# Optimization experiments

Hardware: AMD Instinct MI355X
Metric: run time of the kernel (lower is better)

The kernel has to match this reference:

```python
import jax, jax.numpy as jnp
import numpy as np

NEG_SLOPE = 0.01  # nn.LeakyReLU default

N = 100000
E = 1600000
D_IN = 128
D_OUT = 128


def setup_inputs() -> dict:
    key = jax.random.key(0)
    ks = jax.random.split(key, 8)
    features = jax.random.normal(ks[0], (N, D_IN), dtype=jnp.float32)
    adj_rows = jax.random.randint(ks[1], (E,), 0, N, dtype=jnp.int64)
    adj_cols = jax.random.randint(ks[2], (E,), 0, N, dtype=jnp.int64)
    adj_vals = jax.random.uniform(ks[3], (E,), dtype=jnp.float32)
    s1 = 1.0 / np.sqrt(D_IN)
    W1 = jax.random.uniform(ks[4], (D_IN, D_OUT), jnp.float32, -s1, s1)
    b1 = jax.random.uniform(ks[5], (D_OUT,), jnp.float32, -s1, s1)
    W2 = jax.random.uniform(ks[6], (D_IN, D_OUT), jnp.float32, -s1, s1)
    b2 = jax.random.uniform(ks[7], (D_OUT,), jnp.float32, -s1, s1)
    return {"features": features, "adj_rows": adj_rows, "adj_cols": adj_cols,
            "adj_vals": adj_vals, "W1": W1, "b1": b1, "W2": W2, "b2": b2}


def reference(features, adj_rows, adj_cols, adj_vals, W1, b1, W2, b2):
    # h_neigh = adj @ features  (COO SpMM via gather + segment_sum)
    msgs = adj_vals[:, None] * features[adj_cols]          # [E, D_IN]
    h_neigh = jax.ops.segment_sum(msgs, adj_rows, num_segments=features.shape[0])
    term1 = (features + h_neigh) @ W1 + b1                 # W1(features + h_neigh)
    term2 = (features * h_neigh) @ W2 + b2                 # W2(features * h_neigh)
    pre = term1 + term2
    return jnp.where(pre >= 0, pre, NEG_SLOPE * pre)       # leaky_relu
```

## Files before the change

### kernel.cpp

```cpp
#include <hip/hip_runtime.h>

#define D 128
#define BM 64

typedef short short8 __attribute__((ext_vector_type(8)));
typedef unsigned short ushort8_t __attribute__((ext_vector_type(8)));
typedef float f32x4 __attribute__((ext_vector_type(4)));

__device__ __forceinline__ unsigned short f2bf(float x) {
    unsigned u = __float_as_uint(x);
    unsigned r = (u + 0x7fffu + ((u >> 16) & 1u)) >> 16;
    return (unsigned short)r;
}
__device__ __forceinline__ float bf2f(unsigned short u) {
    return __uint_as_float(((unsigned)u) << 16);
}

__global__ __launch_bounds__(256) void fconv_kernel(
    const float4* __restrict__ feat4, ushort4* __restrict__ fbf4, int total)
{
    int i = blockIdx.x * 256 + threadIdx.x;
    if (i < total) {
        float4 v = feat4[i];
        fbf4[i] = make_ushort4(f2bf(v.x), f2bf(v.y), f2bf(v.z), f2bf(v.w));
    }
}

__global__ __launch_bounds__(256) void wconv_kernel(
    const float* __restrict__ W1, const float* __restrict__ W2,
    unsigned short* __restrict__ WT)
{
    int idx = blockIdx.x * 256 + threadIdx.x;
    int c = idx & 127;
    int k = idx >> 7;
    float w = (k < 128) ? W1[k * 128 + c] : W2[(k - 128) * 128 + c];
    WT[c * 256 + k] = f2bf(w);
}


__global__ __launch_bounds__(256) void bucket_hist_kernel(
    const int* __restrict__ rows, int* __restrict__ bcnt, int E, int nb, int epb)
{
    __shared__ int cnt[1024];
    int t = threadIdx.x;
    for (int i = t; i < nb; i += 256) cnt[i] = 0;
    __syncthreads();
    int e0 = blockIdx.x * epb;
    int e1 = e0 + epb; if (e1 > E) e1 = E;
    for (int e = e0 + t; e < e1; e += 256) atomicAdd(&cnt[rows[e] >> 7], 1);
    __syncthreads();
    for (int i = t; i < nb; i += 256)
        if (cnt[i]) atomicAdd(&bcnt[i], cnt[i]);
}

__global__ __launch_bounds__(1024) void bucket_scan_kernel(
    const int* __restrict__ bcnt, int* __restrict__ bstart,
    int* __restrict__ bcur, int nb, int E)
{
    __shared__ int wsum[16];
    int tid = threadIdx.x, lane = tid & 63, wid = tid >> 6;
    int x = (tid < nb) ? bcnt[tid] : 0;
    int v = x;
    #pragma unroll
    for (int off = 1; off < 64; off <<= 1) {
        int y = __shfl_up(v, off, 64);
        if (lane >= off) v += y;
    }
    if (lane == 63) wsum[wid] = v;
    __syncthreads();
    if (wid == 0 && lane < 16) {
        int s = wsum[lane];
        #pragma unroll
        for (int off = 1; off < 16; off <<= 1) {
            int y = __shfl_up(s, off, 64);
            if (lane >= off) s += y;
        }
        wsum[lane] = s;
    }
    __syncthreads();
    int wexcl = wid ? wsum[wid - 1] : 0;
    int excl = wexcl + v - x;
    if (tid < nb) { bstart[tid] = excl; bcur[tid] = excl; }
    if (tid == 0) bstart[nb] = E;
}

__global__ __launch_bounds__(256) void bucket_scatter_kernel(
    const int* __restrict__ rows, const int* __restrict__ cols,
    const float* __restrict__ vals, int* __restrict__ bcur,
    uint2* __restrict__ bsedge, int E, int nb)
{
    __shared__ int cnt[1024];
    __shared__ int base[1024];
    int t = threadIdx.x;
    int e0 = blockIdx.x * 4096;
    for (int i = t; i < nb; i += 256) cnt[i] = 0;
    __syncthreads();
    #pragma unroll
    for (int q = 0; q < 16; ++q) {
        int e = e0 + t + q * 256;
        if (e < E) atomicAdd(&cnt[rows[e] >> 7], 1);
    }
    __syncthreads();
    for (int i = t; i < nb; i += 256) {
        int c = cnt[i];
        if (c) { base[i] = atomicAdd(&bcur[i], c); cnt[i] = 0; }
    }
    __syncthreads();
    #pragma unroll
    for (int q = 0; q < 16; ++q) {
        int e = e0 + t + q * 256;
        if (e < E) {
            int r = rows[e];
            int b = r >> 7;
            int pos = base[b] + atomicAdd(&cnt[b], 1);
            bsedge[pos] = make_uint2(((unsigned)(r & 127) << 17) | (unsigned)cols[e],
                                     __float_as_uint(vals[e]));
        }
    }
}

__global__ __launch_bounds__(256) void bucket_sort_kernel(
    const uint2* __restrict__ bsedge,
    const int* __restrict__ bstart,
    uint2* __restrict__ sedge,
    int* __restrict__ row_start,
    int N, int E)
{
    __shared__ int cnt[128];
    __shared__ int base[128];
    const int b = blockIdx.x;
    const int t = threadIdx.x;
    const int s = bstart[b], e = bstart[b + 1];
    if (t < 128) cnt[t] = 0;
    __syncthreads();
    for (int j = s + t; j < e; j += 256)
        atomicAdd(&cnt[bsedge[j].x >> 17], 1);
    __syncthreads();
    if (t < 64) {
        int c0 = cnt[2 * t], c1 = cnt[2 * t + 1];
        int pair = c0 + c1;
        int v = pair;
        #pragma unroll
        for (int off = 1; off < 64; off <<= 1) {
            int y = __shfl_up(v, off, 64);
            if (t >= off) v += y;
        }
        int excl = v - pair;
        base[2 * t]     = excl;
        base[2 * t + 1] = excl + c0;
        cnt[2 * t] = 0;
        cnt[2 * t + 1] = 0;
    }
    __syncthreads();
    const int r0 = b << 7;
    if (t < 128 && r0 + t < N) row_start[r0 + t] = s + base[t];
    if (b == 0 && t == 0) row_start[N] = E;
    for (int j = s + t; j < e; j += 256) {
        uint2 ed = bsedge[j];
        int rl = ed.x >> 17;
        int p = atomicAdd(&cnt[rl], 1);
        sedge[s + base[rl] + p] = make_uint2(ed.x & 0x1FFFFu, ed.y);
    }
}

__global__ __launch_bounds__(256) void spmm_ab_kernel(
    const float4* __restrict__ feat4,
    const ushort8_t* __restrict__ fbf8,
    const int* __restrict__ row_start,
    const uint2* __restrict__ sedge,
    unsigned char* __restrict__ ambf, int N)
{
    int t = blockIdx.x * 256 + threadIdx.x;
    int row = t >> 4;
    int l   = t & 15;
    if (row >= N) return;

    int s = row_start[row];
    int e = row_start[row + 1];

    float acc[8] = {};
    int j = s;
    for (; j + 1 < e; j += 2) {
        uint2 e0 = sedge[j], e1 = sedge[j + 1];
        float v0 = __uint_as_float(e0.y), v1 = __uint_as_float(e1.y);
        ushort8_t f0 = fbf8[(size_t)e0.x * 16 + l];
        ushort8_t f1 = fbf8[(size_t)e1.x * 16 + l];
        #pragma unroll
        for (int q = 0; q < 8; ++q) {
            acc[q] = fmaf(v0, bf2f(f0[q]), acc[q]);
            acc[q] = fmaf(v1, bf2f(f1[q]), acc[q]);
        }
    }
    if (j < e) {
        uint2 e0 = sedge[j];
        float v = __uint_as_float(e0.y);
        ushort8_t f = fbf8[(size_t)e0.x * 16 + l];
        #pragma unroll
        for (int q = 0; q < 8; ++q) acc[q] = fmaf(v, bf2f(f[q]), acc[q]);
    }

    float4 fa = feat4[(size_t)row * 32 + 2 * l];
    float4 fb = feat4[(size_t)row * 32 + 2 * l + 1];
    float f[8] = { fa.x, fa.y, fa.z, fa.w, fb.x, fb.y, fb.z, fb.w };

    ushort8_t av, mv;
    #pragma unroll
    for (int q = 0; q < 8; ++q) {
        av[q] = f2bf(f[q] + acc[q]);
        mv[q] = f2bf(f[q] * acc[q]);
    }

    int swz = (row & 7) << 4;
    unsigned char* rowp = ambf + (size_t)row * 512;
    *(ushort8_t*)(rowp + ((16 * l) ^ swz))       = av;
    *(ushort8_t*)(rowp + 256 + ((16 * l) ^ swz)) = mv;
}

__global__ __launch_bounds__(256) void mfma_gemm2_kernel(
    const unsigned char* __restrict__ ambf,
    const unsigned short* __restrict__ WT,
    const float* __restrict__ b1, const float* __restrict__ b2,
    float* __restrict__ out, int N)
{
    __shared__ __align__(16) unsigned char am_raw[64 * 512];

    const int tid = threadIdx.x;
    const int block0 = blockIdx.x * BM;

    const short8* src = (const short8*)(ambf + (size_t)block0 * 512);
    short8* dst = (short8*)am_raw;
    #pragma unroll
    for (int it = 0; it < 8; ++it) {
        int idx = tid + it * 256;
        dst[idx] = src[idx];
    }
    __syncthreads();

    const int lane = tid & 63;
    const int w    = tid >> 6;
    const int wr   = w >> 1;
    const int wc   = w & 1;
    const int l15  = lane & 15;
    const int lk   = lane >> 4;
    const int rswz = (l15 & 7) << 4;

    f32x4 acc[2][4] = {};

    const char* WTc = (const char*)WT;
    const unsigned char* arow0 = am_raw + (wr * 32 + l15) * 512;
    const unsigned char* arow1 = arow0 + 16 * 512;

    #pragma unroll
    for (int ks = 0; ks < 8; ++ks) {
        int kbyte = ks * 64 + lk * 16;
        int akoff = kbyte ^ rswz;
        short8 a0 = *(const short8*)(arow0 + akoff);
        short8 a1 = *(const short8*)(arow1 + akoff);
        short8 bfr[4];
        #pragma unroll
        for (int nc = 0; nc < 4; ++nc) {
            int col = wc * 64 + nc * 16 + l15;
            bfr[nc] = *(const short8*)(WTc + col * 512 + kbyte);
        }
        #pragma unroll
        for (int nc = 0; nc < 4; ++nc) {
            acc[0][nc] = __builtin_amdgcn_mfma_f32_16x16x32_bf16(a0, bfr[nc], acc[0][nc], 0, 0, 0);
            acc[1][nc] = __builtin_amdgcn_mfma_f32_16x16x32_bf16(a1, bfr[nc], acc[1][nc], 0, 0, 0);
        }
    }

    #pragma unroll
    for (int nc = 0; nc < 4; ++nc) {
        int col = wc * 64 + nc * 16 + l15;
        float bias = b1[col] + b2[col];
        #pragma unroll
        for (int mr = 0; mr < 2; ++mr) {
            int rbase = block0 + wr * 32 + mr * 16 + lk * 4;
            #pragma unroll
            for (int r = 0; r < 4; ++r) {
                int row = rbase + r;
                if (row < N) {
                    float v = acc[mr][nc][r] + bias;
                    out[row * 128 + col] = (v >= 0.f) ? v : 0.01f * v;
                }
            }
        }
    }
}

__global__ __launch_bounds__(256) void hist_kernel(
    const int* __restrict__ rows, int* __restrict__ counts, int E)
{
    int e = blockIdx.x * 256 + threadIdx.x;
    if (e < E) atomicAdd(&counts[rows[e]], 1);
}

__global__ __launch_bounds__(256) void scan_pass1(
    const int* __restrict__ counts, int* __restrict__ btot, int N)
{
    int tid = threadIdx.x;
    int i = blockIdx.x * 1024 + tid * 4;
    int s = 0;
    if (i + 3 < N) {
        int4 v = *(const int4*)(counts + i);
        s = v.x + v.y + v.z + v.w;
    } else {
        for (int q = 0; q < 4; ++q) if (i + q < N) s += counts[i + q];
    }
    #pragma unroll
    for (int off = 32; off >= 1; off >>= 1) s += __shfl_down(s, off, 64);
    __shared__ int ws[4];
    if ((tid & 63) == 0) ws[tid >> 6] = s;
    __syncthreads();
    if (tid == 0) btot[blockIdx.x] = ws[0] + ws[1] + ws[2] + ws[3];
}

__global__ __launch_bounds__(1024) void scan_pass2(
    const int* __restrict__ btot, int* __restrict__ boff, int nb)
{
    __shared__ int wsum[16];
    int tid = threadIdx.x, lane = tid & 63, wid = tid >> 6;
    int x = (tid < nb) ? btot[tid] : 0;
    int v = x;
    #pragma unroll
    for (int off = 1; off < 64; off <<= 1) {
        int y = __shfl_up(v, off, 64);
        if (lane >= off) v += y;
    }
    if (lane == 63) wsum[wid] = v;
    __syncthreads();
    if (wid == 0 && lane < 16) {
        int s = wsum[lane];
        #pragma unroll
        for (int off = 1; off < 16; off <<= 1) {
            int y = __shfl_up(s, off, 64);
            if (lane >= off) s += y;
        }
        wsum[lane] = s;
    }
    __syncthreads();
    int wexcl = wid ? wsum[wid - 1] : 0;
    if (tid < nb) boff[tid] = wexcl + v - x;
}

__global__ __launch_bounds__(256) void scan_pass3(
    int* __restrict__ row_start, int* __restrict__ cursor,
    const int* __restrict__ boff, int N, int E)
{
    int tid = threadIdx.x;
    int base = blockIdx.x * 1024 + tid * 4;
    int c0 = 0, c1 = 0, c2 = 0, c3 = 0;
    if (base + 3 < N) {
        int4 v = *(const int4*)(row_start + base);
        c0 = v.x; c1 = v.y; c2 = v.z; c3 = v.w;
    } else {
        if (base + 0 < N) c0 = row_start[base + 0];
        if (base + 1 < N) c1 = row_start[base + 1];
        if (base + 2 < N) c2 = row_start[base + 2];
        if (base + 3 < N) c3 = row_start[base + 3];
    }
    int s0 = c0, s1 = s0 + c1, s2 = s1 + c2, s3 = s2 + c3;
    int lane = tid & 63, wid = tid >> 6;
    int v = s3;
    #pragma unroll
    for (int off = 1; off < 64; off <<= 1) {
        int y = __shfl_up(v, off, 64);
        if (lane >= off) v += y;
    }
    __shared__ int ws[4];
    if (lane == 63) ws[wid] = v;
    __syncthreads();
    int wexcl = 0;
    for (int q = 0; q < wid; ++q) wexcl += ws[q];
    int texcl = wexcl + (v - s3) + boff[blockIdx.x];
    int e0 = texcl, e1 = texcl + s0, e2 = texcl + s1, e3 = texcl + s2;
    if (base + 0 < N) { row_start[base + 0] = e0; cursor[base + 0] = e0; }
    if (base + 1 < N) { row_start[base + 1] = e1; cursor[base + 1] = e1; }
    if (base + 2 < N) { row_start[base + 2] = e2; cursor[base + 2] = e2; }
    if (base + 3 < N) { row_start[base + 3] = e3; cursor[base + 3] = e3; }
    if (blockIdx.x == 0 && tid == 0) row_start[N] = E;
}

__global__ __launch_bounds__(256) void scatter_sort_kernel(
    const int* __restrict__ rows, const int* __restrict__ cols,
    const float* __restrict__ vals, int* __restrict__ cursor,
    uint2* __restrict__ sedge, int E)
{
    int e = blockIdx.x * 256 + threadIdx.x;
    if (e < E) {
        int r = rows[e];
        int p = atomicAdd(&cursor[r], 1);
        sedge[p] = make_uint2((unsigned)cols[e], __float_as_uint(vals[e]));
    }
}

__global__ __launch_bounds__(256) void spmm_kernel(
    const float2* __restrict__ feat2,
    const int* __restrict__ row_start,
    const uint2* __restrict__ sedge,
    float2* __restrict__ h2, int N)
{
    int gw = (blockIdx.x * 256 + threadIdx.x) >> 6;
    int lane = threadIdx.x & 63;
    if (gw >= N) return;
    int s = row_start[gw];
    int e = row_start[gw + 1];
    float2 acc = make_float2(0.f, 0.f);
    int j = s;
    for (; j + 1 < e; j += 2) {
        uint2 e0 = sedge[j], e1 = sedge[j + 1];
        float v0 = __uint_as_float(e0.y), v1 = __uint_as_float(e1.y);
        float2 f0 = feat2[(size_t)e0.x * 64 + lane];
        float2 f1 = feat2[(size_t)e1.x * 64 + lane];
        acc.x = fmaf(v0, f0.x, acc.x);
        acc.y = fmaf(v0, f0.y, acc.y);
        acc.x = fmaf(v1, f1.x, acc.x);
        acc.y = fmaf(v1, f1.y, acc.y);
    }
    if (j < e) {
        uint2 e0 = sedge[j];
        float v = __uint_as_float(e0.y);
        float2 f = feat2[(size_t)e0.x * 64 + lane];
        acc.x = fmaf(v, f.x, acc.x);
        acc.y = fmaf(v, f.y, acc.y);
    }
    h2[(size_t)gw * 64 + lane] = acc;
}

__global__ __launch_bounds__(256) void mfma_gemm_kernel(
    const float4* __restrict__ feat4, const float4* __restrict__ h4,
    const unsigned short* __restrict__ WT,
    const float* __restrict__ b1, const float* __restrict__ b2,
    float* __restrict__ out, int N)
{
    __shared__ __align__(16) unsigned char am_raw[64 * 512];
    const int tid = threadIdx.x;
    const int block0 = blockIdx.x * BM;
    #pragma unroll
    for (int it = 0; it < 8; ++it) {
        int idx  = tid + it * 256;
        int node = idx >> 5;
        int p    = idx & 31;
        int g    = block0 + node;
        float4 fv = make_float4(0.f, 0.f, 0.f, 0.f);
        float4 hv = make_float4(0.f, 0.f, 0.f, 0.f);
        if (g < N) { fv = feat4[g * 32 + p]; hv = h4[g * 32 + p]; }
        ushort4 av = make_ushort4(f2bf(fv.x + hv.x), f2bf(fv.y + hv.y),
                                  f2bf(fv.z + hv.z), f2bf(fv.w + hv.w));
        ushort4 mv = make_ushort4(f2bf(fv.x * hv.x), f2bf(fv.y * hv.y),
                                  f2bf(fv.z * hv.z), f2bf(fv.w * hv.w));
        int swz = (node & 7) << 4;
        *(ushort4*)(am_raw + node * 512 + ((p * 8) ^ swz))       = av;
        *(ushort4*)(am_raw + node * 512 + ((256 + p * 8) ^ swz)) = mv;
    }
    __syncthreads();
    const int lane = tid & 63;
    const int w    = tid >> 6;
    const int wr   = w >> 1;
    const int wc   = w & 1;
    const int l15  = lane & 15;
    const int lk   = lane >> 4;
    const int rswz = (l15 & 7) << 4;
    f32x4 acc[2][4] = {};
    const char* WTc = (const char*)WT;
    const unsigned char* arow0 = am_raw + (wr * 32 + l15) * 512;
    const unsigned char* arow1 = arow0 + 16 * 512;
    #pragma unroll
    for (int ks = 0; ks < 8; ++ks) {
        int kbyte = ks * 64 + lk * 16;
        int akoff = kbyte ^ rswz;
        short8 a0 = *(const short8*)(arow0 + akoff);
        short8 a1 = *(const short8*)(arow1 + akoff);
        short8 bfr[4];
        #pragma unroll
        for (int nc = 0; nc < 4; ++nc) {
            int col = wc * 64 + nc * 16 + l15;
            bfr[nc] = *(const short8*)(WTc + col * 512 + kbyte);
        }
        #pragma unroll
        for (int nc = 0; nc < 4; ++nc) {
            acc[0][nc] = __builtin_amdgcn_mfma_f32_16x16x32_bf16(a0, bfr[nc], acc[0][nc], 0, 0, 0);
            acc[1][nc] = __builtin_amdgcn_mfma_f32_16x16x32_bf16(a1, bfr[nc], acc[1][nc], 0, 0, 0);
        }
    }
    #pragma unroll
    for (int nc = 0; nc < 4; ++nc) {
        int col = wc * 64 + nc * 16 + l15;
        float bias = b1[col] + b2[col];
        #pragma unroll
        for (int mr = 0; mr < 2; ++mr) {
            int rbase = block0 + wr * 32 + mr * 16 + lk * 4;
            #pragma unroll
            for (int r = 0; r < 4; ++r) {
                int row = rbase + r;
                if (row < N) {
                    float v = acc[mr][nc][r] + bias;
                    out[row * 128 + col] = (v >= 0.f) ? v : 0.01f * v;
                }
            }
        }
    }
}

__global__ __launch_bounds__(256) void edge_scatter_kernel(
    const float4* __restrict__ feat4, const int* __restrict__ rows,
    const int* __restrict__ cols, const float* __restrict__ vals,
    float* __restrict__ h, int E)
{
    int idx = blockIdx.x * 256 + threadIdx.x;
    if (idx >= E * 32) return;
    int e = idx >> 5;
    int p = idx & 31;
    int r = rows[e];
    int c = cols[e];
    float v = vals[e];
    float4 f = feat4[c * 32 + p];
    float* hr = h + (long long)r * D + p * 4;
    unsafeAtomicAdd(hr + 0, v * f.x);
    unsafeAtomicAdd(hr + 1, v * f.y);
    unsafeAtomicAdd(hr + 2, v * f.z);
    unsafeAtomicAdd(hr + 3, v * f.w);
}

__global__ __launch_bounds__(256) void fused_gemm_kernel(
    const float* __restrict__ feat, const float* __restrict__ h,
    const float* __restrict__ W1, const float* __restrict__ b1,
    const float* __restrict__ W2, const float* __restrict__ b2,
    float* __restrict__ out, int N)
{
    __shared__ float a_lds[BM][D];
    __shared__ float m_lds[BM][D];
    const int tid = threadIdx.x;
    const int block0 = blockIdx.x * BM;
    const float4* feat4 = (const float4*)feat;
    const float4* h4    = (const float4*)h;
    #pragma unroll
    for (int it = 0; it < 8; ++it) {
        int idx  = tid + it * 256;
        int node = idx >> 5;
        int p    = idx & 31;
        int gnode = block0 + node;
        float4 fv = make_float4(0.f, 0.f, 0.f, 0.f);
        float4 hv = make_float4(0.f, 0.f, 0.f, 0.f);
        if (gnode < N) { fv = feat4[gnode * 32 + p]; hv = h4[gnode * 32 + p]; }
        float4 av = make_float4(fv.x + hv.x, fv.y + hv.y, fv.z + hv.z, fv.w + hv.w);
        float4 mv = make_float4(fv.x * hv.x, fv.y * hv.y, fv.z * hv.z, fv.w * hv.w);
        *(float4*)&a_lds[node][p * 4] = av;
        *(float4*)&m_lds[node][p * 4] = mv;
    }
    __syncthreads();
    const int c = tid & 31;
    const int g = tid >> 5;
    float acc[8][4] = {};
    const float4* W1v = (const float4*)W1;
    const float4* W2v = (const float4*)W2;
    for (int k = 0; k < D; ++k) {
        float4 w1 = W1v[k * 32 + c];
        float4 w2 = W2v[k * 32 + c];
        #pragma unroll
        for (int t = 0; t < 8; ++t) {
            float av = a_lds[g + 8 * t][k];
            float mv = m_lds[g + 8 * t][k];
            acc[t][0] = fmaf(av, w1.x, fmaf(mv, w2.x, acc[t][0]));
            acc[t][1] = fmaf(av, w1.y, fmaf(mv, w2.y, acc[t][1]));
            acc[t][2] = fmaf(av, w1.z, fmaf(mv, w2.z, acc[t][2]));
            acc[t][3] = fmaf(av, w1.w, fmaf(mv, w2.w, acc[t][3]));
        }
    }
    float4 bb1 = ((const float4*)b1)[c];
    float4 bb2 = ((const float4*)b2)[c];
    const float bx = bb1.x + bb2.x, by = bb1.y + bb2.y;
    const float bz = bb1.z + bb2.z, bw = bb1.w + bb2.w;
    #pragma unroll
    for (int t = 0; t < 8; ++t) {
        int gnode = block0 + g + 8 * t;
        if (gnode >= N) continue;
        float4 o;
        o.x = acc[t][0] + bx; o.y = acc[t][1] + by;
        o.z = acc[t][2] + bz; o.w = acc[t][3] + bw;
        o.x = (o.x >= 0.f) ? o.x : 0.01f * o.x;
        o.y = (o.y >= 0.f) ? o.y : 0.01f * o.y;
        o.z = (o.z >= 0.f) ? o.z : 0.01f * o.z;
        o.w = (o.w >= 0.f) ? o.w : 0.01f * o.w;
        ((float4*)out)[gnode * 32 + c] = o;
    }
}

extern "C" void kernel_launch(void* const* d_in, const int* in_sizes, int n_in,
                              void* d_out, int out_size, void* d_ws, size_t ws_size,
                              hipStream_t stream) {
    const float* feat = (const float*)d_in[0];
    const int*   rows = (const int*)d_in[1];
    const int*   cols = (const int*)d_in[2];
    const float* vals = (const float*)d_in[3];
    const float* W1   = (const float*)d_in[4];
    const float* b1   = (const float*)d_in[5];
    const float* W2   = (const float*)d_in[6];
    const float* b2   = (const float*)d_in[7];

    const int N = in_sizes[0] / D;
    const int E = in_sizes[1];
    float* out = (float*)d_out;

    const int NBK  = (N + 127) >> 7;
    const int Npad = NBK << 7;

    size_t off = 0;
    unsigned char* ambf = (unsigned char*)d_ws;                    off += (size_t)Npad * 512;
    unsigned short* featbf = (unsigned short*)((char*)d_ws + off); off += (size_t)N * D * 2;
    off = (off + 15) & ~(size_t)15;
    uint2* sedge = (uint2*)((char*)d_ws + off);                    off += (size_t)E * 8;
    unsigned short* WT = (unsigned short*)((char*)d_ws + off);     off += 128 * 256 * 2;
    int* row_start = (int*)((char*)d_ws + off);                    off += (size_t)(N + 1) * 4;
    size_t common = off;

    off = (common + 15) & ~(size_t)15;
    uint2* bsedge = (uint2*)((char*)d_ws + off);                   off += (size_t)E * 8;
    int* bcnt   = (int*)((char*)d_ws + off);                       off += (size_t)NBK * 4;
    int* bstart = (int*)((char*)d_ws + off);                       off += (size_t)(NBK + 1) * 4;
    int* bcur   = (int*)((char*)d_ws + off);                       off += (size_t)NBK * 4;
    size_t need1a = off;

    if (ws_size >= need1a && NBK <= 1024 && N <= (1 << 17)) {
        hipMemsetAsync(bcnt, 0, (size_t)NBK * sizeof(int), stream);
        fconv_kernel<<<(N * 32 + 255) / 256, 256, 0, stream>>>(
            (const float4*)feat, (ushort4*)featbf, N * 32);
        wconv_kernel<<<128, 256, 0, stream>>>(W1, W2, WT);
        int epb = (E + 255) / 256;
        bucket_hist_kernel<<<256, 256, 0, stream>>>(rows, bcnt, E, NBK, epb);
        bucket_scan_kernel<<<1, 1024, 0, stream>>>(bcnt, bstart, bcur, NBK, E);
        bucket_scatter_kernel<<<(E + 4095) / 4096, 256, 0, stream>>>(
            rows, cols, vals, bcur, bsedge, E, NBK);
        bucket_sort_kernel<<<NBK, 256, 0, stream>>>(
            bsedge, bstart, sedge, row_start, N, E);
        spmm_ab_kernel<<<(N * 16 + 255) / 256, 256, 0, stream>>>(
            (const float4*)feat, (const ushort8_t*)featbf, row_start, sedge,
            ambf, N);
        mfma_gemm2_kernel<<<(N + BM - 1) / BM, 256, 0, stream>>>(
            ambf, WT, b1, b2, out, N);
        return;
    }

    const int NB = (N + 1023) / 1024;
    off = (common + 15) & ~(size_t)15;
    int* cursor = (int*)((char*)d_ws + off);                       off += (size_t)N * 4;
    int* btot = (int*)((char*)d_ws + off);                         off += (size_t)NB * 4;
    int* boff = (int*)((char*)d_ws + off);                         off += (size_t)NB * 4;
    size_t need1b = off;

    if (ws_size >= need1b && NB <= 1024) {
        hipMemsetAsync(row_start, 0, (size_t)(N + 1) * sizeof(int), stream);
        fconv_kernel<<<(N * 32 + 255) / 256, 256, 0, stream>>>(
            (const float4*)feat, (ushort4*)featbf, N * 32);
        wconv_kernel<<<128, 256, 0, stream>>>(W1, W2, WT);
        hist_kernel<<<(E + 255) / 256, 256, 0, stream>>>(rows, row_start, E);
        scan_pass1<<<NB, 256, 0, stream>>>(row_start, btot, N);
        scan_pass2<<<1, 1024, 0, stream>>>(btot, boff, NB);
        scan_pass3<<<NB, 256, 0, stream>>>(row_start, cursor, boff, N, E);
        scatter_sort_kernel<<<(E + 255) / 256, 256, 0, stream>>>(
            rows, cols, vals, cursor, sedge, E);
        spmm_ab_kernel<<<(N * 16 + 255) / 256, 256, 0, stream>>>(
            (const float4*)feat, (const ushort8_t*)featbf, row_start, sedge,
            ambf, N);
        mfma_gemm2_kernel<<<(N + BM - 1) / BM, 256, 0, stream>>>(
            ambf, WT, b1, b2, out, N);
        return;
    }

    off = 0;
    float* h = (float*)d_ws;                           off += (size_t)N * D * 4;
    int* row_start2 = (int*)((char*)d_ws + off);       off += (size_t)(N + 1) * 4;
    int* cursor2    = (int*)((char*)d_ws + off);       off += (size_t)N * 4;
    off = (off + 15) & ~(size_t)15;
    uint2* sedge2   = (uint2*)((char*)d_ws + off);     off += (size_t)E * 8;
    off = (off + 15) & ~(size_t)15;
    unsigned short* WT2 = (unsigned short*)((char*)d_ws + off); off += 128 * 256 * 2;
    int* btot2 = (int*)((char*)d_ws + off);            off += (size_t)NB * 4;
    int* boff2 = (int*)((char*)d_ws + off);            off += (size_t)NB * 4;
    size_t need2 = off;

    if (ws_size >= need2 && NB <= 1024) {
        hipMemsetAsync(row_start2, 0, (size_t)(N + 1) * sizeof(int), stream);
        wconv_kernel<<<128, 256, 0, stream>>>(W1, W2, WT2);
        hist_kernel<<<(E + 255) / 256, 256, 0, stream>>>(rows, row_start2, E);
        scan_pass1<<<NB, 256, 0, stream>>>(row_start2, btot2, N);
        scan_pass2<<<1, 1024, 0, stream>>>(btot2, boff2, NB);
        scan_pass3<<<NB, 256, 0, stream>>>(row_start2, cursor2, boff2, N, E);
        scatter_sort_kernel<<<(E + 255) / 256, 256, 0, stream>>>(
            rows, cols, vals, cursor2, sedge2, E);
        spmm_kernel<<<(N * 64 + 255) / 256, 256, 0, stream>>>(
            (const float2*)feat, row_start2, sedge2, (float2*)h, N);
        mfma_gemm_kernel<<<(N + BM - 1) / BM, 256, 0, stream>>>(
            (const float4*)feat, (const float4*)h, WT2, b1, b2, out, N);
        return;
    }

    size_t hbytes = (size_t)N * D * sizeof(float);
    float* hh = (ws_size >= hbytes) ? (float*)d_ws : out;
    hipMemsetAsync(hh, 0, hbytes, stream);
    edge_scatter_kernel<<<((size_t)E * 32 + 255) / 256, 256, 0, stream>>>(
        (const float4*)feat, rows, cols, vals, hh, E);
    fused_gemm_kernel<<<(N + BM - 1) / BM, 256, 0, stream>>>(
        feat, hh, W1, b1, W2, b2, out, N);
}
```

Measured before the change: 200.4 us.

## Fuse SpMM aggregation with MFMA GEMM epilogue through shared memory

```diff
diff --git a/kernel.cpp b/kernel.cpp
--- a/kernel.cpp
+++ b/kernel.cpp
@@ -160,6 +160,125 @@
         int rl = ed.x >> 17;
         int p = atomicAdd(&cnt[rl], 1);
         sedge[s + base[rl] + p] = make_uint2(ed.x & 0x1FFFFu, ed.y);
+    }
+}
+
+__global__ __launch_bounds__(256) void spmm_gemm_kernel(
+    const float4* __restrict__ feat4,
+    const ushort8_t* __restrict__ fbf8,
+    const int* __restrict__ row_start,
+    const uint2* __restrict__ sedge,
+    const unsigned short* __restrict__ WT,
+    const float* __restrict__ b1, const float* __restrict__ b2,
+    float* __restrict__ out, int N)
+{
+    __shared__ __align__(16) unsigned char am_raw[64 * 512];
+
+    const int tid = threadIdx.x;
+    const int block0 = blockIdx.x * BM;
+    const int rq = tid >> 4;
+    const int l  = tid & 15;
+
+    for (int it = 0; it < 4; ++it) {
+        int node = it * 16 + rq;
+        int row = block0 + node;
+        float acc[8] = {};
+        float f[8] = {};
+        if (row < N) {
+            int s = row_start[row];
+            int e = row_start[row + 1];
+            int j = s;
+            for (; j + 3 < e; j += 4) {
+                uint2 e0 = sedge[j],     e1 = sedge[j + 1];
+                uint2 e2 = sedge[j + 2], e3 = sedge[j + 3];
+                ushort8_t f0 = fbf8[(size_t)e0.x * 16 + l];
+                ushort8_t f1 = fbf8[(size_t)e1.x * 16 + l];
+                ushort8_t f2 = fbf8[(size_t)e2.x * 16 + l];
+                ushort8_t f3 = fbf8[(size_t)e3.x * 16 + l];
+                float v0 = __uint_as_float(e0.y), v1 = __uint_as_float(e1.y);
+                float v2 = __uint_as_float(e2.y), v3 = __uint_as_float(e3.y);
+                #pragma unroll
+                for (int q = 0; q < 8; ++q) {
+                    acc[q] = fmaf(v0, bf2f(f0[q]), acc[q]);
+                    acc[q] = fmaf(v1, bf2f(f1[q]), acc[q]);
+                    acc[q] = fmaf(v2, bf2f(f2[q]), acc[q]);
+                    acc[q] = fmaf(v3, bf2f(f3[q]), acc[q]);
+                }
+            }
+            for (; j < e; ++j) {
+                uint2 e0 = sedge[j];
+                float v = __uint_as_float(e0.y);
+                ushort8_t f0 = fbf8[(size_t)e0.x * 16 + l];
+                #pragma unroll
+                for (int q = 0; q < 8; ++q) acc[q] = fmaf(v, bf2f(f0[q]), acc[q]);
+            }
+            float4 fa = feat4[(size_t)row * 32 + 2 * l];
+            float4 fb = feat4[(size_t)row * 32 + 2 * l + 1];
+            f[0] = fa.x; f[1] = fa.y; f[2] = fa.z; f[3] = fa.w;
+            f[4] = fb.x; f[5] = fb.y; f[6] = fb.z; f[7] = fb.w;
+        }
+        ushort8_t av, mv;
+        #pragma unroll
+        for (int q = 0; q < 8; ++q) {
+            av[q] = f2bf(f[q] + acc[q]);
+            mv[q] = f2bf(f[q] * acc[q]);
+        }
+        int swz = (node & 7) << 4;
+        unsigned char* rowp = am_raw + node * 512;
+        *(ushort8_t*)(rowp + ((16 * l) ^ swz))       = av;
+        *(ushort8_t*)(rowp + 256 + ((16 * l) ^ swz)) = mv;
+    }
+    __syncthreads();
+
+    const int lane = tid & 63;
+    const int w    = tid >> 6;
+    const int wr   = w >> 1;
+    const int wc   = w & 1;
+    const int l15  = lane & 15;
+    const int lk   = lane >> 4;
+    const int rswz = (l15 & 7) << 4;
+
+    f32x4 gacc[2][4] = {};
+
+    const char* WTc = (const char*)WT;
+    const unsigned char* arow0 = am_raw + (wr * 32 + l15) * 512;
+    const unsigned char* arow1 = arow0 + 16 * 512;
+
+    #pragma unroll
+    for (int ks = 0; ks < 8; ++ks) {
+        int kbyte = ks * 64 + lk * 16;
+        int akoff = kbyte ^ rswz;
+        short8 a0 = *(const short8*)(arow0 + akoff);
+        short8 a1 = *(const short8*)(arow1 + akoff);
+        short8 bfr[4];
+        #pragma unroll
+        for (int nc = 0; nc < 4; ++nc) {
+            int col = wc * 64 + nc * 16 + l15;
+            bfr[nc] = *(const short8*)(WTc + col * 512 + kbyte);
+        }
+        #pragma unroll
+        for (int nc = 0; nc < 4; ++nc) {
+            gacc[0][nc] = __builtin_amdgcn_mfma_f32_16x16x32_bf16(a0, bfr[nc], gacc[0][nc], 0, 0, 0);
+            gacc[1][nc] = __builtin_amdgcn_mfma_f32_16x16x32_bf16(a1, bfr[nc], gacc[1][nc], 0, 0, 0);
+        }
+    }
+
+    #pragma unroll
+    for (int nc = 0; nc < 4; ++nc) {
+        int col = wc * 64 + nc * 16 + l15;
+        float bias = b1[col] + b2[col];
+        #pragma unroll
+        for (int mr = 0; mr < 2; ++mr) {
+            int rbase = block0 + wr * 32 + mr * 16 + lk * 4;
+            #pragma unroll
+            for (int r = 0; r < 4; ++r) {
+                int row = rbase + r;
+                if (row < N) {
+                    float v = gacc[mr][nc][r] + bias;
+                    out[row * 128 + col] = (v >= 0.f) ? v : 0.01f * v;
+                }
+            }
+        }
     }
 }
 
@@ -606,15 +725,12 @@
     const int Npad = NBK << 7;
 
     size_t off = 0;
-    unsigned char* ambf = (unsigned char*)d_ws;                    off += (size_t)Npad * 512;
-    unsigned short* featbf = (unsigned short*)((char*)d_ws + off); off += (size_t)N * D * 2;
+    unsigned short* featbf = (unsigned short*)d_ws;                off += (size_t)N * D * 2;
     off = (off + 15) & ~(size_t)15;
     uint2* sedge = (uint2*)((char*)d_ws + off);                    off += (size_t)E * 8;
     unsigned short* WT = (unsigned short*)((char*)d_ws + off);     off += 128 * 256 * 2;
     int* row_start = (int*)((char*)d_ws + off);                    off += (size_t)(N + 1) * 4;
-    size_t common = off;
-
-    off = (common + 15) & ~(size_t)15;
+    off = (off + 15) & ~(size_t)15;
     uint2* bsedge = (uint2*)((char*)d_ws + off);                   off += (size_t)E * 8;
     int* bcnt   = (int*)((char*)d_ws + off);                       off += (size_t)NBK * 4;
     int* bstart = (int*)((char*)d_ws + off);                       off += (size_t)(NBK + 1) * 4;
@@ -633,16 +749,21 @@
             rows, cols, vals, bcur, bsedge, E, NBK);
         bucket_sort_kernel<<<NBK, 256, 0, stream>>>(
             bsedge, bstart, sedge, row_start, N, E);
-        spmm_ab_kernel<<<(N * 16 + 255) / 256, 256, 0, stream>>>(
+        spmm_gemm_kernel<<<(N + BM - 1) / BM, 256, 0, stream>>>(
             (const float4*)feat, (const ushort8_t*)featbf, row_start, sedge,
-            ambf, N);
-        mfma_gemm2_kernel<<<(N + BM - 1) / BM, 256, 0, stream>>>(
-            ambf, WT, b1, b2, out, N);
+            WT, b1, b2, out, N);
         return;
     }
 
     const int NB = (N + 1023) / 1024;
-    off = (common + 15) & ~(size_t)15;
+    off = 0;
+    unsigned char* ambf = (unsigned char*)d_ws;                    off += (size_t)Npad * 512;
+    featbf = (unsigned short*)((char*)d_ws + off);                 off += (size_t)N * D * 2;
+    off = (off + 15) & ~(size_t)15;
+    sedge = (uint2*)((char*)d_ws + off);                           off += (size_t)E * 8;
+    WT = (unsigned short*)((char*)d_ws + off);                     off += 128 * 256 * 2;
+    row_start = (int*)((char*)d_ws + off);                         off += (size_t)(N + 1) * 4;
+    off = (off + 15) & ~(size_t)15;
     int* cursor = (int*)((char*)d_ws + off);                       off += (size_t)N * 4;
     int* btot = (int*)((char*)d_ws + off);                         off += (size_t)NB * 4;
     int* boff = (int*)((char*)d_ws + off);                         off += (size_t)NB * 4;
```

New measurement: 191.8 us. 1.04x faster.

## Fuse feature/weight conversion with bucket histogram; unroll SpMM gather by four

Applied to the files above, without the earlier changes.

```diff
diff --git a/kernel.cpp b/kernel.cpp
--- a/kernel.cpp
+++ b/kernel.cpp
@@ -14,6 +14,41 @@
 }
 __device__ __forceinline__ float bf2f(unsigned short u) {
     return __uint_as_float(((unsigned)u) << 16);
+}
+
+__global__ __launch_bounds__(256) void prep_kernel(
+    const float4* __restrict__ feat4, ushort4* __restrict__ fbf4, int nf4,
+    const float* __restrict__ W1, const float* __restrict__ W2,
+    unsigned short* __restrict__ WT,
+    const int* __restrict__ rows, int* __restrict__ bcnt,
+    int E, int nb, int epb)
+{
+    __shared__ int cnt[1024];
+    const int t = threadIdx.x;
+    const int b = blockIdx.x;
+    for (int i = t; i < nb; i += 256) cnt[i] = 0;
+    __syncthreads();
+
+    int e0 = b * epb;
+    int e1 = e0 + epb; if (e1 > E) e1 = E;
+    for (int e = e0 + t; e < e1; e += 256) atomicAdd(&cnt[rows[e] >> 7], 1);
+
+    for (int i = b * 256 + t; i < nf4; i += 256 * 256) {
+        float4 v = feat4[i];
+        fbf4[i] = make_ushort4(f2bf(v.x), f2bf(v.y), f2bf(v.z), f2bf(v.w));
+    }
+
+    if (b < 128) {
+        int idx = b * 256 + t;
+        int c = idx & 127;
+        int k = idx >> 7;
+        float w = (k < 128) ? W1[k * 128 + c] : W2[(k - 128) * 128 + c];
+        WT[c * 256 + k] = f2bf(w);
+    }
+
+    __syncthreads();
+    for (int i = t; i < nb; i += 256)
+        if (cnt[i]) atomicAdd(&bcnt[i], cnt[i]);
 }
 
 __global__ __launch_bounds__(256) void fconv_kernel(
@@ -35,22 +70,6 @@
     int k = idx >> 7;
     float w = (k < 128) ? W1[k * 128 + c] : W2[(k - 128) * 128 + c];
     WT[c * 256 + k] = f2bf(w);
-}
-
-
-__global__ __launch_bounds__(256) void bucket_hist_kernel(
-    const int* __restrict__ rows, int* __restrict__ bcnt, int E, int nb, int epb)
-{
-    __shared__ int cnt[1024];
-    int t = threadIdx.x;
-    for (int i = t; i < nb; i += 256) cnt[i] = 0;
-    __syncthreads();
-    int e0 = blockIdx.x * epb;
-    int e1 = e0 + epb; if (e1 > E) e1 = E;
-    for (int e = e0 + t; e < e1; e += 256) atomicAdd(&cnt[rows[e] >> 7], 1);
-    __syncthreads();
-    for (int i = t; i < nb; i += 256)
-        if (cnt[i]) atomicAdd(&bcnt[i], cnt[i]);
 }
 
 __global__ __launch_bounds__(1024) void bucket_scan_kernel(
@@ -164,7 +183,6 @@
 }
 
 __global__ __launch_bounds__(256) void spmm_ab_kernel(
-    const float4* __restrict__ feat4,
     const ushort8_t* __restrict__ fbf8,
     const int* __restrict__ row_start,
     const uint2* __restrict__ sedge,
@@ -180,34 +198,38 @@
 
     float acc[8] = {};
     int j = s;
-    for (; j + 1 < e; j += 2) {
-        uint2 e0 = sedge[j], e1 = sedge[j + 1];
-        float v0 = __uint_as_float(e0.y), v1 = __uint_as_float(e1.y);
+    for (; j + 3 < e; j += 4) {
+        uint2 e0 = sedge[j],     e1 = sedge[j + 1];
+        uint2 e2 = sedge[j + 2], e3 = sedge[j + 3];
         ushort8_t f0 = fbf8[(size_t)e0.x * 16 + l];
         ushort8_t f1 = fbf8[(size_t)e1.x * 16 + l];
+        ushort8_t f2 = fbf8[(size_t)e2.x * 16 + l];
+        ushort8_t f3 = fbf8[(size_t)e3.x * 16 + l];
+        float v0 = __uint_as_float(e0.y), v1 = __uint_as_float(e1.y);
+        float v2 = __uint_as_float(e2.y), v3 = __uint_as_float(e3.y);
         #pragma unroll
         for (int q = 0; q < 8; ++q) {
             acc[q] = fmaf(v0, bf2f(f0[q]), acc[q]);
             acc[q] = fmaf(v1, bf2f(f1[q]), acc[q]);
-        }
-    }
-    if (j < e) {
+            acc[q] = fmaf(v2, bf2f(f2[q]), acc[q]);
+            acc[q] = fmaf(v3, bf2f(f3[q]), acc[q]);
+        }
+    }
+    for (; j < e; ++j) {
         uint2 e0 = sedge[j];
         float v = __uint_as_float(e0.y);
-        ushort8_t f = fbf8[(size_t)e0.x * 16 + l];
-        #pragma unroll
-        for (int q = 0; q < 8; ++q) acc[q] = fmaf(v, bf2f(f[q]), acc[q]);
-    }
-
-    float4 fa = feat4[(size_t)row * 32 + 2 * l];
-    float4 fb = feat4[(size_t)row * 32 + 2 * l + 1];
-    float f[8] = { fa.x, fa.y, fa.z, fa.w, fb.x, fb.y, fb.z, fb.w };
-
+        ushort8_t f0 = fbf8[(size_t)e0.x * 16 + l];
+        #pragma unroll
+        for (int q = 0; q < 8; ++q) acc[q] = fmaf(v, bf2f(f0[q]), acc[q]);
+    }
+
+    ushort8_t fown = fbf8[(size_t)row * 16 + l];
     ushort8_t av, mv;
     #pragma unroll
     for (int q = 0; q < 8; ++q) {
-        av[q] = f2bf(f[q] + acc[q]);
-        mv[q] = f2bf(f[q] * acc[q]);
+        float f = bf2f(fown[q]);
+        av[q] = f2bf(f + acc[q]);
+        mv[q] = f2bf(f * acc[q]);
     }
 
     int swz = (row & 7) << 4;
@@ -612,9 +634,7 @@
     uint2* sedge = (uint2*)((char*)d_ws + off);                    off += (size_t)E * 8;
     unsigned short* WT = (unsigned short*)((char*)d_ws + off);     off += 128 * 256 * 2;
     int* row_start = (int*)((char*)d_ws + off);                    off += (size_t)(N + 1) * 4;
-    size_t common = off;
-
-    off = (common + 15) & ~(size_t)15;
+    off = (off + 15) & ~(size_t)15;
     uint2* bsedge = (uint2*)((char*)d_ws + off);                   off += (size_t)E * 8;
     int* bcnt   = (int*)((char*)d_ws + off);                       off += (size_t)NBK * 4;
     int* bstart = (int*)((char*)d_ws + off);                       off += (size_t)(NBK + 1) * 4;
@@ -623,26 +643,31 @@
 
     if (ws_size >= need1a && NBK <= 1024 && N <= (1 << 17)) {
         hipMemsetAsync(bcnt, 0, (size_t)NBK * sizeof(int), stream);
-        fconv_kernel<<<(N * 32 + 255) / 256, 256, 0, stream>>>(
-            (const float4*)feat, (ushort4*)featbf, N * 32);
-        wconv_kernel<<<128, 256, 0, stream>>>(W1, W2, WT);
         int epb = (E + 255) / 256;
-        bucket_hist_kernel<<<256, 256, 0, stream>>>(rows, bcnt, E, NBK, epb);
+        prep_kernel<<<256, 256, 0, stream>>>(
+            (const float4*)feat, (ushort4*)featbf, N * 32,
+            W1, W2, WT, rows, bcnt, E, NBK, epb);
         bucket_scan_kernel<<<1, 1024, 0, stream>>>(bcnt, bstart, bcur, NBK, E);
         bucket_scatter_kernel<<<(E + 4095) / 4096, 256, 0, stream>>>(
             rows, cols, vals, bcur, bsedge, E, NBK);
         bucket_sort_kernel<<<NBK, 256, 0, stream>>>(
             bsedge, bstart, sedge, row_start, N, E);
         spmm_ab_kernel<<<(N * 16 + 255) / 256, 256, 0, stream>>>(
-            (const float4*)feat, (const ushort8_t*)featbf, row_start, sedge,
-            ambf, N);
+            (const ushort8_t*)featbf, row_start, sedge, ambf, N);
         mfma_gemm2_kernel<<<(N + BM - 1) / BM, 256, 0, stream>>>(
             ambf, WT, b1, b2, out, N);
         return;
     }
 
     const int NB = (N + 1023) / 1024;
-    off = (common + 15) & ~(size_t)15;
+    off = 0;
+    ambf = (unsigned char*)d_ws;                                   off += (size_t)Npad * 512;
+    featbf = (unsigned short*)((char*)d_ws + off);                 off += (size_t)N * D * 2;
+    off = (off + 15) & ~(size_t)15;
+    sedge = (uint2*)((char*)d_ws + off);                           off += (size_t)E * 8;
+    WT = (unsigned short*)((char*)d_ws + off);                     off += 128 * 256 * 2;
+    row_start = (int*)((char*)d_ws + off);                         off += (size_t)(N + 1) * 4;
+    off = (off + 15) & ~(size_t)15;
     int* cursor = (int*)((char*)d_ws + off);                       off += (size_t)N * 4;
     int* btot = (int*)((char*)d_ws + off);                         off += (size_t)NB * 4;
     int* boff = (int*)((char*)d_ws + off);                         off += (size_t)NB * 4;
@@ -660,8 +685,7 @@
         scatter_sort_kernel<<<(E + 255) / 256, 256, 0, stream>>>(
             rows, cols, vals, cursor, sedge, E);
         spmm_ab_kernel<<<(N * 16 + 255) / 256, 256, 0, stream>>>(
-            (const float4*)feat, (const ushort8_t*)featbf, row_start, sedge,
-            ambf, N);
+            (const ushort8_t*)featbf, row_start, sedge, ambf, N);
         mfma_gemm2_kernel<<<(N + BM - 1) / BM, 256, 0, stream>>>(
             ambf, WT, b1, b2, out, N);
         return;
```

Result: faster. 193.0 us (-3.7%).
